# Kernel tuning notes

Hardware: AMD Instinct MI355X
Metric: run time of the kernel (lower is better)

The kernel has to match this reference:

```python
import jax, jax.numpy as jnp
import numpy as np

N = 100000
IN_C = 128
HID_C = 128
OUT_C = 128
E = 3200000


def setup_inputs() -> dict:
    key = jax.random.key(0)
    ks = jax.random.split(key, 8)
    x = jax.random.normal(ks[0], (N, IN_C), dtype=jnp.float32)
    edge_index = jax.random.randint(ks[1], (2, E), 0, N, dtype=jnp.int64)
    edge_weight = jnp.ones((E,), dtype=jnp.float32)
    s = 1.0 / np.sqrt(HID_C)
    W_conv = jax.random.uniform(ks[2], (HID_C, IN_C), jnp.float32, -s, s)
    b_conv = jnp.zeros((HID_C,), dtype=jnp.float32)
    W_fc = jax.random.uniform(ks[3], (HID_C, HID_C), jnp.float32, -s, s)
    b_fc = jax.random.uniform(ks[4], (HID_C,), jnp.float32, -s, s)
    W_fc2 = jax.random.uniform(ks[5], (OUT_C, HID_C), jnp.float32, -s, s)
    b_fc2 = jax.random.uniform(ks[6], (OUT_C,), jnp.float32, -s, s)
    return {"x": x, "edge_index": edge_index, "edge_weight": edge_weight,
            "W_conv": W_conv, "b_conv": b_conv, "W_fc": W_fc, "b_fc": b_fc,
            "W_fc2": W_fc2, "b_fc2": b_fc2}


def _gcn_conv(x, edge_index, edge_weight, W_conv, b_conv):
    n = x.shape[0]
    # add self-loops with weight 1 (PyG GCNConv default)
    loop = jnp.arange(n, dtype=edge_index.dtype)
    src = jnp.concatenate([edge_index[0], loop])
    dst = jnp.concatenate([edge_index[1], loop])
    ew = jnp.concatenate([edge_weight, jnp.ones((n,), dtype=edge_weight.dtype)])
    # symmetric normalization: deg^-1/2[src] * w * deg^-1/2[dst]
    deg = jax.ops.segment_sum(ew, dst, num_segments=n)
    dinv = jnp.where(deg > 0, jax.lax.rsqrt(jnp.where(deg > 0, deg, 1.0)), 0.0)
    norm = dinv[src] * ew * dinv[dst]  # [E+N]
    h = x @ W_conv.T                   # [N, hid], bias-free linear first
    msg = h[src] * norm[:, None]       # gather + scale
    agg = jax.ops.segment_sum(msg, dst, num_segments=n)  # scatter-add
    return agg + b_conv


def reference(x, edge_index, edge_weight, W_conv, b_conv, W_fc, b_fc, W_fc2, b_fc2):
    h = _gcn_conv(x, edge_index, edge_weight, W_conv, b_conv)
    h = jax.nn.relu(h)
    h = jax.nn.relu(h @ W_fc.T + b_fc)
    return h @ W_fc2.T + b_fc2
```

## Files before the change

kernel.cpp:

```cpp
#include <hip/hip_runtime.h>

typedef short bf16x8 __attribute__((ext_vector_type(8)));
typedef float f32x4 __attribute__((ext_vector_type(4)));

#define PS 64
#define PMAX 2048
#define CAPP 2432
#define NB 256

__device__ __forceinline__ unsigned short f2bf(float f) {
    unsigned int u = __float_as_uint(f);
    u = (u + 0x7FFFu + ((u >> 16) & 1u)) >> 16;
    return (unsigned short)u;
}

__global__ __launch_bounds__(1024) void scat_k(const int* __restrict__ ei,
                                               const float* __restrict__ ew,
                                               int* __restrict__ partCnt,
                                               int2* __restrict__ regions,
                                               int E, int P, int EPB) {
    __shared__ int cntl[PMAX];
    __shared__ int basel[PMAX];
    const int b = blockIdx.x, tid = threadIdx.x;
    for (int i = tid; i < P; i += 1024) cntl[i] = 0;
    __syncthreads();
    const int s = b * EPB, e = min(E, s + EPB);
    for (int i = s + tid; i < e; i += 1024)
        atomicAdd(&cntl[ei[E + i] >> 6], 1);
    __syncthreads();
    for (int p = tid; p < P; p += 1024) {
        int c = cntl[p];
        basel[p] = p * CAPP + (c ? atomicAdd(&partCnt[p], c) : 0);
        cntl[p] = 0;
    }
    __syncthreads();
    for (int i = s + tid; i < e; i += 1024) {
        int src = ei[i];
        int dst = ei[E + i];
        float w = ew[i];
        int p = dst >> 6, dl = dst & 63;
        int lidx = atomicAdd(&cntl[p], 1);
        int pos = basel[p] + lidx;
        if (pos < (p + 1) * CAPP)
            regions[pos] = make_int2(src | (dl << 24), __float_as_int(w));
    }
}

__global__ __launch_bounds__(256) void dgemm1_k(const float* __restrict__ x,
                                                const float* __restrict__ Wc,
                                                const int* __restrict__ partCnt,
                                                const int2* __restrict__ regions,
                                                float* __restrict__ dinv,
                                                int* __restrict__ nodeOff,
                                                unsigned short* __restrict__ h,
                                                int M, int P) {
    __shared__ __align__(16) unsigned short Wl[128 * 136];
    __shared__ float degl[256];
    __shared__ int cl[256];
    const int tid = threadIdx.x;
    degl[tid] = 0.f; cl[tid] = 0;

#pragma unroll
    for (int i = 0; i < 16; ++i) {
        int e4 = i * 256 + tid;
        float4 v = ((const float4*)Wc)[e4];
        int e = e4 * 4, r = e >> 7, cc = e & 127;
        unsigned short* pp = &Wl[r * 136 + cc];
        pp[0] = f2bf(v.x); pp[1] = f2bf(v.y); pp[2] = f2bf(v.z); pp[3] = f2bf(v.w);
    }
    __syncthreads();

#pragma unroll
    for (int q = 0; q < 4; ++q) {
        int p = blockIdx.x * 4 + q;
        if (p < P) {
            const int cnt = min(partCnt[p], CAPP);
            const int2* reg = regions + (size_t)p * CAPP;
            for (int i = tid; i < cnt; i += 256) {
                int2 r = reg[i];
                int dl = q * 64 + ((r.x >> 24) & 63);
                atomicAdd(&cl[dl], 1);
                atomicAdd(&degl[dl], __int_as_float(r.y));
            }
        }
    }
    __syncthreads();
    {
        int lane = tid & 63;
        int cn = cl[tid];
        int v = cn;
#pragma unroll
        for (int off = 1; off < 64; off <<= 1) {
            int u = __shfl_up(v, off, 64);
            if (lane >= off) v += u;
        }
        int node = blockIdx.x * 256 + tid;
        float d = rsqrtf(1.0f + degl[tid]);
        if (node < M) { nodeOff[node] = v - cn; dinv[node] = d; }
        degl[tid] = d;
    }
    __syncthreads();

    const int wave = tid >> 6, lane = tid & 63;
    const int m = lane & 15, quad = lane >> 4;

#pragma unroll
    for (int t = 0; t < 4; ++t) {
        const int tileBase = blockIdx.x * 256 + t * 64;
        if (tileBase >= M) break;
        const int rowBase = tileBase + wave * 16;
        int arow = rowBase + m;
        int arowc = arow < M ? arow : (M - 1);

        bf16x8 afrag[4];
        const float* pa = x + (size_t)arowc * 128 + quad * 8;
#pragma unroll
        for (int kc = 0; kc < 4; ++kc) {
            float4 v0 = *(const float4*)(pa + kc * 32);
            float4 v1 = *(const float4*)(pa + kc * 32 + 4);
            bf16x8 f;
            f[0] = (short)f2bf(v0.x); f[1] = (short)f2bf(v0.y);
            f[2] = (short)f2bf(v0.z); f[3] = (short)f2bf(v0.w);
            f[4] = (short)f2bf(v1.x); f[5] = (short)f2bf(v1.y);
            f[6] = (short)f2bf(v1.z); f[7] = (short)f2bf(v1.w);
            afrag[kc] = f;
        }

        float dv[4];
#pragma unroll
        for (int r = 0; r < 4; ++r)
            dv[r] = degl[t * 64 + wave * 16 + quad * 4 + r];

#pragma unroll
        for (int nt = 0; nt < 8; ++nt) {
            f32x4 acc = {0.f, 0.f, 0.f, 0.f};
            const unsigned short* wb = &Wl[(nt * 16 + m) * 136 + quad * 8];
#pragma unroll
            for (int kc = 0; kc < 4; ++kc) {
                bf16x8 bfrag = *(const bf16x8*)(wb + kc * 32);
                acc = __builtin_amdgcn_mfma_f32_16x16x32_bf16(afrag[kc], bfrag, acc, 0, 0, 0);
            }
            const int col = nt * 16 + m;
#pragma unroll
            for (int r = 0; r < 4; ++r) {
                int row = rowBase + quad * 4 + r;
                if (row < M)
                    h[(size_t)row * 128 + col] = f2bf(acc[r] * dv[r]);
            }
        }
    }
}

__global__ __launch_bounds__(256) void aggF_k(const int* __restrict__ partCnt,
                                              const int* __restrict__ nodeOff,
                                              const int2* __restrict__ regions,
                                              const unsigned short* __restrict__ h,
                                              const float* __restrict__ dinv,
                                              const float* __restrict__ bconv,
                                              unsigned short* __restrict__ h2, int N) {
    __shared__ __align__(16) int2 stag[CAPP];
    __shared__ int cstart[PS + 1];
    __shared__ int wcur[PS];
    const int p = blockIdx.x, tid = threadIdx.x;
    const int cnt = min(partCnt[p], CAPP);
    const int2* reg = regions + (size_t)p * CAPP;

    if (tid < PS) {
        int node = p * PS + tid;
        int o = (node < N) ? nodeOff[node] : cnt;
        cstart[tid] = o;
        wcur[tid] = o;
    } else if (tid == PS) {
        cstart[PS] = cnt;
    }
    __syncthreads();
    for (int i = tid; i < cnt; i += 256) {
        int2 r = reg[i];
        int pos = atomicAdd(&wcur[(r.x >> 24) & 63], 1);
        stag[pos] = r;
    }
    __syncthreads();

    const int wave = tid >> 6, lane = tid & 63;
    const int g = lane >> 4;
    const int c8 = (lane & 15) * 8;
    for (int nl = wave; nl < PS; nl += 4) {
        int n = p * PS + nl;
        if (n >= N) continue;
        const int s = cstart[nl], e = cstart[nl + 1];
        float acc[8] = {0.f, 0.f, 0.f, 0.f, 0.f, 0.f, 0.f, 0.f};
        int j = s;
        const int efull = s + ((e - s) & ~15);
        for (; j < efull; j += 16) {
            int2 r0 = stag[j + g];
            int2 r1 = stag[j + 4 + g];
            int2 r2 = stag[j + 8 + g];
            int2 r3 = stag[j + 12 + g];
            float w0 = __int_as_float(r0.y), w1 = __int_as_float(r1.y);
            float w2 = __int_as_float(r2.y), w3 = __int_as_float(r3.y);
            int4 q0 = *(const int4*)(h + (((unsigned)r0.x & 0xFFFFFFu) << 7) + c8);
            int4 q1 = *(const int4*)(h + (((unsigned)r1.x & 0xFFFFFFu) << 7) + c8);
            int4 q2 = *(const int4*)(h + (((unsigned)r2.x & 0xFFFFFFu) << 7) + c8);
            int4 q3 = *(const int4*)(h + (((unsigned)r3.x & 0xFFFFFFu) << 7) + c8);
#pragma unroll
            for (int d = 0; d < 4; ++d) {
                unsigned ud = ((const unsigned*)&q0)[d];
                acc[2 * d]     += __uint_as_float(ud << 16) * w0;
                acc[2 * d + 1] += __uint_as_float(ud & 0xFFFF0000u) * w0;
            }
#pragma unroll
            for (int d = 0; d < 4; ++d) {
                unsigned ud = ((const unsigned*)&q1)[d];
                acc[2 * d]     += __uint_as_float(ud << 16) * w1;
                acc[2 * d + 1] += __uint_as_float(ud & 0xFFFF0000u) * w1;
            }
#pragma unroll
            for (int d = 0; d < 4; ++d) {
                unsigned ud = ((const unsigned*)&q2)[d];
                acc[2 * d]     += __uint_as_float(ud << 16) * w2;
                acc[2 * d + 1] += __uint_as_float(ud & 0xFFFF0000u) * w2;
            }
#pragma unroll
            for (int d = 0; d < 4; ++d) {
                unsigned ud = ((const unsigned*)&q3)[d];
                acc[2 * d]     += __uint_as_float(ud << 16) * w3;
                acc[2 * d + 1] += __uint_as_float(ud & 0xFFFF0000u) * w3;
            }
        }
        for (; j < e; j += 8) {
            int j0 = j + g, j1 = j + 4 + g;
            int2 r0 = stag[j0 < e ? j0 : s];
            int2 r1 = stag[j1 < e ? j1 : s];
            float w0 = (j0 < e) ? __int_as_float(r0.y) : 0.f;
            float w1 = (j1 < e) ? __int_as_float(r1.y) : 0.f;
            int4 q0 = *(const int4*)(h + (((unsigned)r0.x & 0xFFFFFFu) << 7) + c8);
            int4 q1 = *(const int4*)(h + (((unsigned)r1.x & 0xFFFFFFu) << 7) + c8);
#pragma unroll
            for (int d = 0; d < 4; ++d) {
                unsigned ud = ((const unsigned*)&q0)[d];
                acc[2 * d]     += __uint_as_float(ud << 16) * w0;
                acc[2 * d + 1] += __uint_as_float(ud & 0xFFFF0000u) * w0;
            }
#pragma unroll
            for (int d = 0; d < 4; ++d) {
                unsigned ud = ((const unsigned*)&q1)[d];
                acc[2 * d]     += __uint_as_float(ud << 16) * w1;
                acc[2 * d + 1] += __uint_as_float(ud & 0xFFFF0000u) * w1;
            }
        }
#pragma unroll
        for (int k = 0; k < 8; ++k) {
            float v = acc[k];
            v += __shfl_xor(v, 16, 64);
            v += __shfl_xor(v, 32, 64);
            acc[k] = v;
        }
        if (g == 0) {
            float di = dinv[n];
            int4 qs = *(const int4*)(h + ((unsigned)n << 7) + c8);
            float4 b0 = *(const float4*)(bconv + c8);
            float4 b1 = *(const float4*)(bconv + c8 + 4);
            float bb[8] = {b0.x, b0.y, b0.z, b0.w, b1.x, b1.y, b1.z, b1.w};
            bf16x8 o;
#pragma unroll
            for (int d = 0; d < 4; ++d) {
                unsigned ud = ((const unsigned*)&qs)[d];
                float h0 = __uint_as_float(ud << 16);
                float h1 = __uint_as_float(ud & 0xFFFF0000u);
                o[2 * d]     = (short)f2bf(fmaxf(di * (acc[2 * d] + h0) + bb[2 * d], 0.f));
                o[2 * d + 1] = (short)f2bf(fmaxf(di * (acc[2 * d + 1] + h1) + bb[2 * d + 1], 0.f));
            }
            *(bf16x8*)(h2 + (size_t)n * 128 + c8) = o;
        }
    }
}

__global__ __launch_bounds__(256) void gemm23_k(const unsigned short* __restrict__ h2,
                                                const float* __restrict__ Wf,
                                                const float* __restrict__ bfc,
                                                const float* __restrict__ W2,
                                                const float* __restrict__ b2,
                                                float* __restrict__ out, int M) {
    __shared__ __align__(16) unsigned short Wl[128 * 136];
    __shared__ __align__(16) unsigned short Tl[64 * 136];
    const int tid = threadIdx.x;

#pragma unroll
    for (int i = 0; i < 16; ++i) {
        int e4 = i * 256 + tid;
        float4 v = ((const float4*)Wf)[e4];
        int e = e4 * 4, r = e >> 7, cc = e & 127;
        unsigned short* pp = &Wl[r * 136 + cc];
        pp[0] = f2bf(v.x); pp[1] = f2bf(v.y); pp[2] = f2bf(v.z); pp[3] = f2bf(v.w);
    }
    __syncthreads();

    const int wave = tid >> 6, lane = tid & 63;
    const int m = lane & 15, quad = lane >> 4;
    const int rowBase = blockIdx.x * 64 + wave * 16;
    int arow = rowBase + m;
    int arowc = arow < M ? arow : (M - 1);

    bf16x8 afrag[4];
    {
        const unsigned short* pa = h2 + (size_t)arowc * 128 + quad * 8;
#pragma unroll
        for (int kc = 0; kc < 4; ++kc)
            afrag[kc] = *(const bf16x8*)(pa + kc * 32);
    }

#pragma unroll
    for (int nt = 0; nt < 8; ++nt) {
        f32x4 acc = {0.f, 0.f, 0.f, 0.f};
        const unsigned short* wb = &Wl[(nt * 16 + m) * 136 + quad * 8];
#pragma unroll
        for (int kc = 0; kc < 4; ++kc) {
            bf16x8 bfrag = *(const bf16x8*)(wb + kc * 32);
            acc = __builtin_amdgcn_mfma_f32_16x16x32_bf16(afrag[kc], bfrag, acc, 0, 0, 0);
        }
        const int col = nt * 16 + m;
        float bv = bfc[col];
#pragma unroll
        for (int r = 0; r < 4; ++r) {
            int rowl = wave * 16 + quad * 4 + r;
            Tl[rowl * 136 + col] = f2bf(fmaxf(acc[r] + bv, 0.f));
        }
    }
    __syncthreads();

#pragma unroll
    for (int i = 0; i < 16; ++i) {
        int e4 = i * 256 + tid;
        float4 v = ((const float4*)W2)[e4];
        int e = e4 * 4, r = e >> 7, cc = e & 127;
        unsigned short* pp = &Wl[r * 136 + cc];
        pp[0] = f2bf(v.x); pp[1] = f2bf(v.y); pp[2] = f2bf(v.z); pp[3] = f2bf(v.w);
    }
    __syncthreads();

    bf16x8 afrag2[4];
    {
        const unsigned short* pa = &Tl[(wave * 16 + m) * 136 + quad * 8];
#pragma unroll
        for (int kc = 0; kc < 4; ++kc)
            afrag2[kc] = *(const bf16x8*)(pa + kc * 32);
    }
#pragma unroll
    for (int nt = 0; nt < 8; ++nt) {
        f32x4 acc = {0.f, 0.f, 0.f, 0.f};
        const unsigned short* wb = &Wl[(nt * 16 + m) * 136 + quad * 8];
#pragma unroll
        for (int kc = 0; kc < 4; ++kc) {
            bf16x8 bfrag = *(const bf16x8*)(wb + kc * 32);
            acc = __builtin_amdgcn_mfma_f32_16x16x32_bf16(afrag2[kc], bfrag, acc, 0, 0, 0);
        }
        const int col = nt * 16 + m;
        float bv = b2[col];
#pragma unroll
        for (int r = 0; r < 4; ++r) {
            int row = rowBase + quad * 4 + r;
            if (row < M)
                out[(size_t)row * 128 + col] = acc[r] + bv;
        }
    }
}

extern "C" void kernel_launch(void* const* d_in, const int* in_sizes, int n_in,
                              void* d_out, int out_size, void* d_ws, size_t ws_size,
                              hipStream_t stream) {
    const float* x  = (const float*)d_in[0];
    const int* ei   = (const int*)d_in[1];
    const float* ew = (const float*)d_in[2];
    const float* Wc = (const float*)d_in[3];
    const float* bc = (const float*)d_in[4];
    const float* Wf = (const float*)d_in[5];
    const float* bf = (const float*)d_in[6];
    const float* W2 = (const float*)d_in[7];
    const float* b2 = (const float*)d_in[8];
    float* out = (float*)d_out;

    const int N = in_sizes[0] / 128;
    const int E = in_sizes[2];
    const int P = (N + PS - 1) / PS;

    auto align256 = [](size_t v) { return (v + 255) & ~(size_t)255; };
    char* ws = (char*)d_ws;
    size_t off = 0;
    float* dinv  = (float*)(ws + off); off += align256((size_t)N * 4);
    int* nodeOff = (int*)(ws + off);   off += align256((size_t)N * 4);
    int* partCnt = (int*)(ws + off);   off += align256((size_t)P * 4);
    unsigned short* h  = (unsigned short*)(ws + off); off += (size_t)N * 256;
    unsigned short* h2 = (unsigned short*)(ws + off);

    int2* regions = (int2*)out;

    const int EPB = (E + NB - 1) / NB;

    hipMemsetAsync(partCnt, 0, (size_t)P * 4, stream);
    scat_k<<<NB, 1024, 0, stream>>>(ei, ew, partCnt, regions, E, P, EPB);
    dgemm1_k<<<(N + 255) / 256, 256, 0, stream>>>(x, Wc, partCnt, regions, dinv, nodeOff, h, N, P);
    aggF_k<<<P, 256, 0, stream>>>(partCnt, nodeOff, regions, h, dinv, bc, h2, N);
    gemm23_k<<<(N + 63) / 64, 256, 0, stream>>>(h2, Wf, bf, W2, b2, out, N);
}
```

Measured before the change: 386.9 us.

## Split h into two 64-column halves and aggregate each half separately

The first GEMM now writes h in a column-split layout: two contiguous [N,64] bf16 planes instead of one [N,128] array. The aggregation kernel makes two passes over each partition's edges, gathering 128-byte rows from one half-plane at a time. The aim is a smaller gather working set per pass, so more of it fits in L2/MALL and random row gathers hit cache more often. The cost is reading the staged edge list twice and doing twice as many gathers, each half as wide.

```diff
diff --git a/kernel.cpp b/kernel.cpp
--- a/kernel.cpp
+++ b/kernel.cpp
@@ -1,6 +1,7 @@
 #include <hip/hip_runtime.h>
 
 typedef short bf16x8 __attribute__((ext_vector_type(8)));
+typedef short bf16x4 __attribute__((ext_vector_type(4)));
 typedef float f32x4 __attribute__((ext_vector_type(4)));
 
 #define PS 64
@@ -145,7 +146,7 @@
             for (int r = 0; r < 4; ++r) {
                 int row = rowBase + quad * 4 + r;
                 if (row < M)
-                    h[(size_t)row * 128 + col] = f2bf(acc[r] * dv[r]);
+                    h[((size_t)(col >> 6) * M + row) * 64 + (col & 63)] = f2bf(acc[r] * dv[r]);
             }
         }
     }
@@ -183,94 +184,100 @@
 
     const int wave = tid >> 6, lane = tid & 63;
     const int g = lane >> 4;
-    const int c8 = (lane & 15) * 8;
-    for (int nl = wave; nl < PS; nl += 4) {
-        int n = p * PS + nl;
-        if (n >= N) continue;
-        const int s = cstart[nl], e = cstart[nl + 1];
-        float acc[8] = {0.f, 0.f, 0.f, 0.f, 0.f, 0.f, 0.f, 0.f};
-        int j = s;
-        const int efull = s + ((e - s) & ~15);
-        for (; j < efull; j += 16) {
-            int2 r0 = stag[j + g];
-            int2 r1 = stag[j + 4 + g];
-            int2 r2 = stag[j + 8 + g];
-            int2 r3 = stag[j + 12 + g];
-            float w0 = __int_as_float(r0.y), w1 = __int_as_float(r1.y);
-            float w2 = __int_as_float(r2.y), w3 = __int_as_float(r3.y);
-            int4 q0 = *(const int4*)(h + (((unsigned)r0.x & 0xFFFFFFu) << 7) + c8);
-            int4 q1 = *(const int4*)(h + (((unsigned)r1.x & 0xFFFFFFu) << 7) + c8);
-            int4 q2 = *(const int4*)(h + (((unsigned)r2.x & 0xFFFFFFu) << 7) + c8);
-            int4 q3 = *(const int4*)(h + (((unsigned)r3.x & 0xFFFFFFu) << 7) + c8);
-#pragma unroll
-            for (int d = 0; d < 4; ++d) {
-                unsigned ud = ((const unsigned*)&q0)[d];
-                acc[2 * d]     += __uint_as_float(ud << 16) * w0;
-                acc[2 * d + 1] += __uint_as_float(ud & 0xFFFF0000u) * w0;
-            }
-#pragma unroll
-            for (int d = 0; d < 4; ++d) {
-                unsigned ud = ((const unsigned*)&q1)[d];
-                acc[2 * d]     += __uint_as_float(ud << 16) * w1;
-                acc[2 * d + 1] += __uint_as_float(ud & 0xFFFF0000u) * w1;
-            }
-#pragma unroll
-            for (int d = 0; d < 4; ++d) {
-                unsigned ud = ((const unsigned*)&q2)[d];
-                acc[2 * d]     += __uint_as_float(ud << 16) * w2;
-                acc[2 * d + 1] += __uint_as_float(ud & 0xFFFF0000u) * w2;
-            }
-#pragma unroll
-            for (int d = 0; d < 4; ++d) {
-                unsigned ud = ((const unsigned*)&q3)[d];
-                acc[2 * d]     += __uint_as_float(ud << 16) * w3;
-                acc[2 * d + 1] += __uint_as_float(ud & 0xFFFF0000u) * w3;
-            }
-        }
-        for (; j < e; j += 8) {
-            int j0 = j + g, j1 = j + 4 + g;
-            int2 r0 = stag[j0 < e ? j0 : s];
-            int2 r1 = stag[j1 < e ? j1 : s];
-            float w0 = (j0 < e) ? __int_as_float(r0.y) : 0.f;
-            float w1 = (j1 < e) ? __int_as_float(r1.y) : 0.f;
-            int4 q0 = *(const int4*)(h + (((unsigned)r0.x & 0xFFFFFFu) << 7) + c8);
-            int4 q1 = *(const int4*)(h + (((unsigned)r1.x & 0xFFFFFFu) << 7) + c8);
-#pragma unroll
-            for (int d = 0; d < 4; ++d) {
-                unsigned ud = ((const unsigned*)&q0)[d];
-                acc[2 * d]     += __uint_as_float(ud << 16) * w0;
-                acc[2 * d + 1] += __uint_as_float(ud & 0xFFFF0000u) * w0;
-            }
-#pragma unroll
-            for (int d = 0; d < 4; ++d) {
-                unsigned ud = ((const unsigned*)&q1)[d];
-                acc[2 * d]     += __uint_as_float(ud << 16) * w1;
-                acc[2 * d + 1] += __uint_as_float(ud & 0xFFFF0000u) * w1;
-            }
-        }
-#pragma unroll
-        for (int k = 0; k < 8; ++k) {
-            float v = acc[k];
-            v += __shfl_xor(v, 16, 64);
-            v += __shfl_xor(v, 32, 64);
-            acc[k] = v;
-        }
-        if (g == 0) {
-            float di = dinv[n];
-            int4 qs = *(const int4*)(h + ((unsigned)n << 7) + c8);
-            float4 b0 = *(const float4*)(bconv + c8);
-            float4 b1 = *(const float4*)(bconv + c8 + 4);
-            float bb[8] = {b0.x, b0.y, b0.z, b0.w, b1.x, b1.y, b1.z, b1.w};
-            bf16x8 o;
-#pragma unroll
-            for (int d = 0; d < 4; ++d) {
-                unsigned ud = ((const unsigned*)&qs)[d];
-                float h0 = __uint_as_float(ud << 16);
-                float h1 = __uint_as_float(ud & 0xFFFF0000u);
-                o[2 * d]     = (short)f2bf(fmaxf(di * (acc[2 * d] + h0) + bb[2 * d], 0.f));
-                o[2 * d + 1] = (short)f2bf(fmaxf(di * (acc[2 * d + 1] + h1) + bb[2 * d + 1], 0.f));
-            }
-            *(bf16x8*)(h2 + (size_t)n * 128 + c8) = o;
+    const int c4 = (lane & 15) * 4;
+
+#pragma unroll
+    for (int hh = 0; hh < 2; ++hh) {
+        const unsigned short* hb = h + ((size_t)hh * (size_t)N << 6);
+        for (int nl = wave; nl < PS; nl += 4) {
+            int n = p * PS + nl;
+            if (n >= N) continue;
+            const int s = cstart[nl], e = cstart[nl + 1];
+            float acc[4] = {0.f, 0.f, 0.f, 0.f};
+            int j = s;
+            const int efull = s + ((e - s) & ~15);
+            for (; j < efull; j += 16) {
+                int2 r0 = stag[j + g];
+                int2 r1 = stag[j + 4 + g];
+                int2 r2 = stag[j + 8 + g];
+                int2 r3 = stag[j + 12 + g];
+                float w0 = __int_as_float(r0.y), w1 = __int_as_float(r1.y);
+                float w2 = __int_as_float(r2.y), w3 = __int_as_float(r3.y);
+                int2 q0 = *(const int2*)(hb + ((((unsigned)r0.x & 0xFFFFFFu)) << 6) + c4);
+                int2 q1 = *(const int2*)(hb + ((((unsigned)r1.x & 0xFFFFFFu)) << 6) + c4);
+                int2 q2 = *(const int2*)(hb + ((((unsigned)r2.x & 0xFFFFFFu)) << 6) + c4);
+                int2 q3 = *(const int2*)(hb + ((((unsigned)r3.x & 0xFFFFFFu)) << 6) + c4);
+                {
+                    unsigned ux = (unsigned)q0.x, uy = (unsigned)q0.y;
+                    acc[0] += __uint_as_float(ux << 16) * w0;
+                    acc[1] += __uint_as_float(ux & 0xFFFF0000u) * w0;
+                    acc[2] += __uint_as_float(uy << 16) * w0;
+                    acc[3] += __uint_as_float(uy & 0xFFFF0000u) * w0;
+                }
+                {
+                    unsigned ux = (unsigned)q1.x, uy = (unsigned)q1.y;
+                    acc[0] += __uint_as_float(ux << 16) * w1;
+                    acc[1] += __uint_as_float(ux & 0xFFFF0000u) * w1;
+                    acc[2] += __uint_as_float(uy << 16) * w1;
+                    acc[3] += __uint_as_float(uy & 0xFFFF0000u) * w1;
+                }
+                {
+                    unsigned ux = (unsigned)q2.x, uy = (unsigned)q2.y;
+                    acc[0] += __uint_as_float(ux << 16) * w2;
+                    acc[1] += __uint_as_float(ux & 0xFFFF0000u) * w2;
+                    acc[2] += __uint_as_float(uy << 16) * w2;
+                    acc[3] += __uint_as_float(uy & 0xFFFF0000u) * w2;
+                }
+                {
+                    unsigned ux = (unsigned)q3.x, uy = (unsigned)q3.y;
+                    acc[0] += __uint_as_float(ux << 16) * w3;
+                    acc[1] += __uint_as_float(ux & 0xFFFF0000u) * w3;
+                    acc[2] += __uint_as_float(uy << 16) * w3;
+                    acc[3] += __uint_as_float(uy & 0xFFFF0000u) * w3;
+                }
+            }
+            for (; j < e; j += 8) {
+                int j0 = j + g, j1 = j + 4 + g;
+                int2 r0 = stag[j0 < e ? j0 : s];
+                int2 r1 = stag[j1 < e ? j1 : s];
+                float w0 = (j0 < e) ? __int_as_float(r0.y) : 0.f;
+                float w1 = (j1 < e) ? __int_as_float(r1.y) : 0.f;
+                int2 q0 = *(const int2*)(hb + ((((unsigned)r0.x & 0xFFFFFFu)) << 6) + c4);
+                int2 q1 = *(const int2*)(hb + ((((unsigned)r1.x & 0xFFFFFFu)) << 6) + c4);
+                {
+                    unsigned ux = (unsigned)q0.x, uy = (unsigned)q0.y;
+                    acc[0] += __uint_as_float(ux << 16) * w0;
+                    acc[1] += __uint_as_float(ux & 0xFFFF0000u) * w0;
+                    acc[2] += __uint_as_float(uy << 16) * w0;
+                    acc[3] += __uint_as_float(uy & 0xFFFF0000u) * w0;
+                }
+                {
+                    unsigned ux = (unsigned)q1.x, uy = (unsigned)q1.y;
+                    acc[0] += __uint_as_float(ux << 16) * w1;
+                    acc[1] += __uint_as_float(ux & 0xFFFF0000u) * w1;
+                    acc[2] += __uint_as_float(uy << 16) * w1;
+                    acc[3] += __uint_as_float(uy & 0xFFFF0000u) * w1;
+                }
+            }
+#pragma unroll
+            for (int k = 0; k < 4; ++k) {
+                float v = acc[k];
+                v += __shfl_xor(v, 16, 64);
+                v += __shfl_xor(v, 32, 64);
+                acc[k] = v;
+            }
+            if (g == 0) {
+                float di = dinv[n];
+                int2 qs = *(const int2*)(hb + ((size_t)(unsigned)n << 6) + c4);
+                float4 b = *(const float4*)(bconv + hh * 64 + c4);
+                unsigned ux = (unsigned)qs.x, uy = (unsigned)qs.y;
+                bf16x4 o;
+                o[0] = (short)f2bf(fmaxf(di * (acc[0] + __uint_as_float(ux << 16)) + b.x, 0.f));
+                o[1] = (short)f2bf(fmaxf(di * (acc[1] + __uint_as_float(ux & 0xFFFF0000u)) + b.y, 0.f));
+                o[2] = (short)f2bf(fmaxf(di * (acc[2] + __uint_as_float(uy << 16)) + b.z, 0.f));
+                o[3] = (short)f2bf(fmaxf(di * (acc[3] + __uint_as_float(uy & 0xFFFF0000u)) + b.w, 0.f));
+                *(bf16x4*)(h2 + (size_t)n * 128 + hh * 64 + c4) = o;
+            }
         }
     }
 }
```

After: 372.3 us. 3.8% less time.
